# Kernel tuning notes

Hardware: AMD Instinct MI355X
Metric: run time of the kernel (lower is better)

The kernel has to match this reference:

```python
import jax, jax.numpy as jnp
import numpy as np

B, S, D, IDX = 4, 4096, 1024, 64
W = 128          # window_size
STRIDE = 64      # stride (<= W, so every query position is covered)
SPARSE = 0.5     # sparse_ratio


def setup_inputs() -> dict:
    key = jax.random.key(0)
    k1, k2, k3 = jax.random.split(key, 3)
    x = jax.random.normal(k1, (B, S, D), jnp.float32)
    wq = jax.random.normal(k2, (IDX, D), jnp.float32) * 0.02  # q_proj weight [out,in]
    wk = jax.random.normal(k3, (IDX, D), jnp.float32) * 0.02  # k_proj weight [out,in]
    return {"x": x, "wq": wq, "wk": wk}


def reference(x, wq, wk):
    # Faithful vectorization of SlidingWindowPattern.forward.
    # For every visited (start, q) pair in the original nested loops,
    # key_end = q+1 and key_start = max(0, q-W+1) are independent of `start`,
    # so the union of scatter writes equals ONE windowed top-k per query q
    # with k = max(1, int(min(q+1, W) * sparse_ratio)).
    B_, S_, _ = x.shape
    dt = x.dtype
    q = jnp.einsum('bsd,ed->bse', x, wq)
    k = jnp.einsum('bsd,ed->bse', x, wk)
    scores = jax.nn.relu(jnp.einsum('bqe,bke->bqk', q, k))  # [B,S,S]

    qpos = jnp.arange(S_)                                   # [S]
    j = jnp.arange(W)                                       # [W]
    key_idx = qpos[:, None] - (W - 1) + j[None, :]          # [S,W] absolute key positions
    valid = key_idx >= 0                                    # window is [max(0,q-W+1), q]

    gather_idx = jnp.broadcast_to(jnp.clip(key_idx, 0, S_ - 1)[None], (B_, S_, W))
    win = jnp.take_along_axis(scores, gather_idx, axis=2)   # [B,S,W]
    win = jnp.where(valid[None], win, -jnp.inf)

    order = jnp.argsort(-win, axis=-1)                      # descending; rank r -> window offset j
    win_len = jnp.minimum(qpos + 1, W)                      # number of valid keys per q
    ksel = jnp.maximum(1, jnp.floor(win_len.astype(jnp.float32) * SPARSE).astype(jnp.int32))  # [S]

    sel_key = qpos[None, :, None] - (W - 1) + order         # [B,S,W] absolute key of rank r
    write = jnp.arange(W)[None, None, :] < ksel[None, :, None]
    tgt = jnp.where(write, sel_key, S_)                     # S_ = out-of-bounds -> dropped

    mask = jnp.full((B_, S_, S_), -jnp.inf, dtype=dt)
    mask = mask.at[jnp.arange(B_)[:, None, None],
                   jnp.arange(S_)[None, :, None],
                   tgt].set(jnp.zeros((), dt), mode='drop')
    return mask[:, None]                                    # [B,1,S,S]
```

## Files before the change

### kernel.cpp

```cpp
#include <hip/hip_runtime.h>
#include <cstdint>
#include <cstddef>

#define S_LEN 4096
#define D_DIM 1024
#define NE    64
#define QB    32

typedef short short8 __attribute__((ext_vector_type(8)));
typedef float f32x4  __attribute__((ext_vector_type(4)));

__device__ __forceinline__ unsigned short f2bf(float f) {
    unsigned u = __float_as_uint(f);
    return (unsigned short)((u + 0x7FFFu + ((u >> 16) & 1u)) >> 16);
}

__global__ __launch_bounds__(256) void conv_w(
    const float* __restrict__ wq, const float* __restrict__ wk,
    unsigned short* __restrict__ whi, unsigned short* __restrict__ wlo)
{
    const int g = blockIdx.x * 256 + threadIdx.x;
    const int c = g >> 8;
    const int k = (g & 255) * 4;
    const float* src = (c < NE) ? (wq + (size_t)c * D_DIM + k)
                                : (wk + (size_t)(c - NE) * D_DIM + k);
    const float4 v = *(const float4*)src;
    unsigned short h[4], l[4];
    const float* vf = (const float*)&v;
    #pragma unroll
    for (int i = 0; i < 4; ++i) {
        h[i] = f2bf(vf[i]);
        l[i] = f2bf(vf[i] - __uint_as_float((unsigned)h[i] << 16));
    }
    *(ushort4*)(whi + (size_t)c * D_DIM + k) = make_ushort4(h[0], h[1], h[2], h[3]);
    *(ushort4*)(wlo + (size_t)c * D_DIM + k) = make_ushort4(l[0], l[1], l[2], l[3]);
}

__global__ __launch_bounds__(512) void proj_mfma(
    const float* __restrict__ x,
    const unsigned short* __restrict__ whi, const unsigned short* __restrict__ wlo,
    unsigned int* __restrict__ qhl)
{
    __shared__ __align__(16) short smem[24576];
    short* sxh = smem;
    short* sxl = smem + 4096;
    short* swh = smem + 8192;
    short* swl = smem + 16384;

    const int tid = threadIdx.x;
    const int m0  = blockIdx.x * 64;
    const int wv  = tid >> 6, l = tid & 63;
    const int mp  = wv & 1, np = wv >> 1;
    const int lrow = l & 15, lgrp = l >> 4;
    const int xr = tid >> 3, xg = tid & 7;
    const int wc = tid >> 3, wg = tid & 7;

    f32x4 acc[2][2] = {};

    for (int kb = 0; kb < D_DIM; kb += 64) {
        {
            const float* xs = x + (size_t)(m0 + xr) * D_DIM + kb + 8 * xg;
            const float4 a = *(const float4*)xs;
            const float4 b = *(const float4*)(xs + 4);
            short8 hv, lv;
            const float* af = (const float*)&a;
            const float* bf = (const float*)&b;
            #pragma unroll
            for (int i = 0; i < 4; ++i) {
                const unsigned short h0 = f2bf(af[i]);
                const unsigned short h1 = f2bf(bf[i]);
                hv[i]     = (short)h0;
                hv[i + 4] = (short)h1;
                lv[i]     = (short)f2bf(af[i] - __uint_as_float((unsigned)h0 << 16));
                lv[i + 4] = (short)f2bf(bf[i] - __uint_as_float((unsigned)h1 << 16));
            }
            const int d = xr * 64 + ((xg ^ (xr & 7)) * 8);
            *(short8*)(sxh + d) = hv;
            *(short8*)(sxl + d) = lv;
        }
        #pragma unroll
        for (int p = 0; p < 2; ++p) {
            const int c = wc + 64 * p;
            const size_t srcOff = (size_t)c * D_DIM + kb + 8 * wg;
            const int d = c * 64 + ((wg ^ (c & 7)) * 8);
            *(uint4*)(swh + d) = *(const uint4*)(whi + srcOff);
            *(uint4*)(swl + d) = *(const uint4*)(wlo + srcOff);
        }
        __syncthreads();

        short8 ah[2][2], al[2][2];
        #pragma unroll
        for (int mi = 0; mi < 2; ++mi) {
            const int ar = (2 * mp + mi) * 16 + lrow;
            #pragma unroll
            for (int kc = 0; kc < 2; ++kc) {
                const int g = kc * 4 + lgrp;
                const int o = ar * 64 + ((g ^ (ar & 7)) * 8);
                ah[mi][kc] = *(const short8*)(sxh + o);
                al[mi][kc] = *(const short8*)(sxl + o);
            }
        }
        #pragma unroll
        for (int ni = 0; ni < 2; ++ni) {
            const int bc = (2 * np + ni) * 16 + lrow;
            #pragma unroll
            for (int kc = 0; kc < 2; ++kc) {
                const int g = kc * 4 + lgrp;
                const int o = bc * 64 + ((g ^ (bc & 7)) * 8);
                const short8 bh = *(const short8*)(swh + o);
                const short8 bl = *(const short8*)(swl + o);
                #pragma unroll
                for (int mi = 0; mi < 2; ++mi) {
                    acc[mi][ni] = __builtin_amdgcn_mfma_f32_16x16x32_bf16(
                        ah[mi][kc], bh, acc[mi][ni], 0, 0, 0);
                    acc[mi][ni] = __builtin_amdgcn_mfma_f32_16x16x32_bf16(
                        al[mi][kc], bh, acc[mi][ni], 0, 0, 0);
                    acc[mi][ni] = __builtin_amdgcn_mfma_f32_16x16x32_bf16(
                        ah[mi][kc], bl, acc[mi][ni], 0, 0, 0);
                }
            }
        }
        __syncthreads();
    }

    unsigned int* tb = (unsigned int*)smem;
    #pragma unroll
    for (int mi = 0; mi < 2; ++mi)
        #pragma unroll
        for (int ni = 0; ni < 2; ++ni) {
            const int col = (2 * np + ni) * 16 + lrow;
            const int rb  = (2 * mp + mi) * 16 + lgrp * 4;
            #pragma unroll
            for (int v = 0; v < 4; ++v) {
                const float f = acc[mi][ni][v];
                const unsigned short h = f2bf(f);
                const unsigned short lo = f2bf(f - __uint_as_float((unsigned)h << 16));
                tb[(rb + v) * 128 + col] = ((unsigned)h << 16) | lo;
            }
        }
    __syncthreads();
    const uint4* tb4 = (const uint4*)tb;
    uint4* dst = (uint4*)(qhl + (size_t)m0 * 128);
    #pragma unroll
    for (int p = 0; p < 4; ++p) {
        const int i = tid + 512 * p;
        dst[i] = tb4[i];
    }
}

__global__ __launch_bounds__(512) void swp_sel(
    const unsigned int* __restrict__ qhl, unsigned short* __restrict__ outp)
{
    __shared__ __align__(16) short kmem[2 * 192 * 64];
    __shared__ __align__(16) short qmem[2 * 32 * 64];
    __shared__ __align__(16) unsigned char selb[QB * 16];
    short* kh = kmem;
    short* kl = kmem + 192 * 64;
    short* qh = qmem;
    short* ql = qmem + 32 * 64;
    unsigned long long* skey = (unsigned long long*)kmem;

    const int tid = threadIdx.x;
    const int b   = blockIdx.x >> 7;
    const int s0  = (blockIdx.x & 127) * QB;
    const size_t rowQ = (size_t)b * S_LEN + s0;

    {
        const int r = tid >> 4, c4 = tid & 15;
        const uint4 u = *(const uint4*)(qhl + (rowQ + r) * 128 + 4 * c4);
        const int off = r * 64 + (((c4 >> 1) ^ (r & 7)) * 8) + 4 * (c4 & 1);
        *(short4*)(qh + off) = make_short4((short)(u.x >> 16), (short)(u.y >> 16),
                                           (short)(u.z >> 16), (short)(u.w >> 16));
        *(short4*)(ql + off) = make_short4((short)(u.x & 0xFFFF), (short)(u.y & 0xFFFF),
                                           (short)(u.z & 0xFFFF), (short)(u.w & 0xFFFF));
    }
    #pragma unroll
    for (int p = 0; p < 5; ++p) {
        const int i = tid + 512 * p;
        const int r = i >> 4, c4 = i & 15;
        const int sk = s0 - 127 + r;
        if (r < 159 && sk >= 0) {
            const uint4 u = *(const uint4*)(qhl + ((size_t)b * S_LEN + sk) * 128 + 64 + 4 * c4);
            const int off = r * 64 + (((c4 >> 1) ^ (r & 7)) * 8) + 4 * (c4 & 1);
            *(short4*)(kh + off) = make_short4((short)(u.x >> 16), (short)(u.y >> 16),
                                               (short)(u.z >> 16), (short)(u.w >> 16));
            *(short4*)(kl + off) = make_short4((short)(u.x & 0xFFFF), (short)(u.y & 0xFFFF),
                                               (short)(u.z & 0xFFFF), (short)(u.w & 0xFFFF));
        }
    }
    __syncthreads();

    const int wv = tid >> 6, l = tid & 63;
    const int mi = wv & 1, nbase = 3 * (wv >> 1);
    const int lrow = l & 15, lgrp = l >> 4;
    f32x4 sacc[3] = {};
    {
        short8 ah[2], al[2];
        const int ar = mi * 16 + lrow;
        #pragma unroll
        for (int kc = 0; kc < 2; ++kc) {
            const int g = kc * 4 + lgrp;
            const int o = ar * 64 + ((g ^ (ar & 7)) * 8);
            ah[kc] = *(const short8*)(qh + o);
            al[kc] = *(const short8*)(ql + o);
        }
        #pragma unroll
        for (int nn = 0; nn < 3; ++nn) {
            const int bc = (nbase + nn) * 16 + lrow;
            #pragma unroll
            for (int kc = 0; kc < 2; ++kc) {
                const int g = kc * 4 + lgrp;
                const int o = bc * 64 + ((g ^ (bc & 7)) * 8);
                const short8 bh = *(const short8*)(kh + o);
                const short8 bl = *(const short8*)(kl + o);
                sacc[nn] = __builtin_amdgcn_mfma_f32_16x16x32_bf16(ah[kc], bh, sacc[nn], 0, 0, 0);
                sacc[nn] = __builtin_amdgcn_mfma_f32_16x16x32_bf16(al[kc], bh, sacc[nn], 0, 0, 0);
                sacc[nn] = __builtin_amdgcn_mfma_f32_16x16x32_bf16(ah[kc], bl, sacc[nn], 0, 0, 0);
            }
        }
    }
    __syncthreads();

    const int kvmin = 127 - s0;
    #pragma unroll
    for (int nn = 0; nn < 3; ++nn) {
        const int kidx = (nbase + nn) * 16 + lrow;
        #pragma unroll
        for (int v = 0; v < 4; ++v) {
            const int qi = mi * 16 + lgrp * 4 + v;
            const int jo = kidx - qi;
            if (jo >= 0 && jo <= 127) {
                unsigned long long key = 0ull;
                if (kidx >= kvmin) {
                    const unsigned int bits = __float_as_uint(fmaxf(sacc[nn][v], 0.0f));
                    key = ((unsigned long long)bits << 32) | (unsigned int)(159 - kidx);
                }
                skey[qi * 131 + jo] = key;
            }
        }
    }
    __syncthreads();

    {
        const int qi = tid >> 4, sl = tid & 15;
        unsigned long long th[8];
        #pragma unroll
        for (int m = 0; m < 8; ++m) th[m] = skey[qi * 131 + sl * 8 + m];
        int rk[8] = {};
        #pragma unroll 4
        for (int ii = 0; ii < 128; ++ii) {
            const unsigned long long kx = skey[qi * 131 + ii];
            #pragma unroll
            for (int m = 0; m < 8; ++m) rk[m] += (kx > th[m]) ? 1 : 0;
        }
        const int qpos = s0 + qi;
        const int wl = (qpos + 1 < 128) ? (qpos + 1) : 128;
        const int ks = ((wl >> 1) > 1) ? (wl >> 1) : 1;
        unsigned int mk = 0;
        #pragma unroll
        for (int m = 0; m < 8; ++m) if (rk[m] < ks) mk |= (1u << m);
        selb[qi * 16 + sl] = (unsigned char)mk;
    }
    __syncthreads();

    const int wb = tid >> 6, ln = tid & 63;
    #pragma unroll
    for (int rr = 0; rr < 4; ++rr) {
        const int qi = wb * 4 + rr;
        const int qpos = s0 + qi;
        const int wstart = qpos - 127;
        unsigned short* orow = outp + (rowQ + qi) * (size_t)S_LEN;
        #pragma unroll
        for (int h = 0; h < 2; ++h) {
            const int jo = ln + 64 * h;
            const int col = wstart + jo;
            if (col >= 0) {
                const int bit = (selb[qi * 16 + (jo >> 3)] >> (jo & 7)) & 1;
                orow[col] = bit ? (unsigned short)0u : (unsigned short)0xFBFFu;
            }
        }
    }
}

extern "C" void kernel_launch(void* const* d_in, const int* in_sizes, int n_in,
                              void* d_out, int out_size, void* d_ws, size_t ws_size,
                              hipStream_t stream)
{
    (void)in_sizes; (void)n_in; (void)out_size; (void)ws_size;
    const float* x  = (const float*)d_in[0];
    const float* wq = (const float*)d_in[1];
    const float* wk = (const float*)d_in[2];
    unsigned short* out = (unsigned short*)d_out;

    unsigned int* qhl = (unsigned int*)d_ws;
    unsigned short* whi = (unsigned short*)((char*)d_ws + ((size_t)8 << 20));
    unsigned short* wlo = whi + (size_t)128 * D_DIM;

    conv_w<<<128, 256, 0, stream>>>(wq, wk, whi, wlo);
    proj_mfma<<<256, 512, 0, stream>>>(x, whi, wlo, qhl);
    swp_sel<<<512, 512, 0, stream>>>(qhl, out);
}
```

Before: 61.10 us.

## Fuse weight bf16 split into projection and store q/k as split hi/lo planes

Removes the separate conv_w launch by converting fp32 weights to bf16 hi/lo pairs inside the projection kernel's tile loader. The projection output changes from packed hi|lo words to two separate planes, so the selection kernel can copy 16-byte chunks straight into shared memory without unpacking. It also changes the skey row stride from 131 to 132 and processes two keys per rank-loop iteration. Each projection block now redoes the weight conversion, adding extra ALU work and fp32 weight traffic in exchange for one fewer launch.

```diff
diff --git a/kernel.cpp b/kernel.cpp
--- a/kernel.cpp
+++ b/kernel.cpp
@@ -15,31 +15,10 @@
     return (unsigned short)((u + 0x7FFFu + ((u >> 16) & 1u)) >> 16);
 }
 
-__global__ __launch_bounds__(256) void conv_w(
-    const float* __restrict__ wq, const float* __restrict__ wk,
-    unsigned short* __restrict__ whi, unsigned short* __restrict__ wlo)
-{
-    const int g = blockIdx.x * 256 + threadIdx.x;
-    const int c = g >> 8;
-    const int k = (g & 255) * 4;
-    const float* src = (c < NE) ? (wq + (size_t)c * D_DIM + k)
-                                : (wk + (size_t)(c - NE) * D_DIM + k);
-    const float4 v = *(const float4*)src;
-    unsigned short h[4], l[4];
-    const float* vf = (const float*)&v;
-    #pragma unroll
-    for (int i = 0; i < 4; ++i) {
-        h[i] = f2bf(vf[i]);
-        l[i] = f2bf(vf[i] - __uint_as_float((unsigned)h[i] << 16));
-    }
-    *(ushort4*)(whi + (size_t)c * D_DIM + k) = make_ushort4(h[0], h[1], h[2], h[3]);
-    *(ushort4*)(wlo + (size_t)c * D_DIM + k) = make_ushort4(l[0], l[1], l[2], l[3]);
-}
-
 __global__ __launch_bounds__(512) void proj_mfma(
     const float* __restrict__ x,
-    const unsigned short* __restrict__ whi, const unsigned short* __restrict__ wlo,
-    unsigned int* __restrict__ qhl)
+    const float* __restrict__ wq, const float* __restrict__ wk,
+    unsigned short* __restrict__ qhi, unsigned short* __restrict__ qlo)
 {
     __shared__ __align__(16) short smem[24576];
     short* sxh = smem;
@@ -81,10 +60,24 @@
         #pragma unroll
         for (int p = 0; p < 2; ++p) {
             const int c = wc + 64 * p;
-            const size_t srcOff = (size_t)c * D_DIM + kb + 8 * wg;
+            const float* wsrc = (p ? wk : wq) + (size_t)wc * D_DIM + kb + 8 * wg;
+            const float4 a = *(const float4*)wsrc;
+            const float4 b = *(const float4*)(wsrc + 4);
+            short8 hv, lv;
+            const float* af = (const float*)&a;
+            const float* bf = (const float*)&b;
+            #pragma unroll
+            for (int i = 0; i < 4; ++i) {
+                const unsigned short h0 = f2bf(af[i]);
+                const unsigned short h1 = f2bf(bf[i]);
+                hv[i]     = (short)h0;
+                hv[i + 4] = (short)h1;
+                lv[i]     = (short)f2bf(af[i] - __uint_as_float((unsigned)h0 << 16));
+                lv[i + 4] = (short)f2bf(bf[i] - __uint_as_float((unsigned)h1 << 16));
+            }
             const int d = c * 64 + ((wg ^ (c & 7)) * 8);
-            *(uint4*)(swh + d) = *(const uint4*)(whi + srcOff);
-            *(uint4*)(swl + d) = *(const uint4*)(wlo + srcOff);
+            *(short8*)(swh + d) = hv;
+            *(short8*)(swl + d) = lv;
         }
         __syncthreads();
 
@@ -140,16 +133,24 @@
         }
     __syncthreads();
     const uint4* tb4 = (const uint4*)tb;
-    uint4* dst = (uint4*)(qhl + (size_t)m0 * 128);
     #pragma unroll
     for (int p = 0; p < 4; ++p) {
         const int i = tid + 512 * p;
-        dst[i] = tb4[i];
+        const uint4 u = tb4[i];
+        const int row = i >> 5, c4 = (i & 31) * 4;
+        const size_t off = (size_t)(m0 + row) * 128 + c4;
+        *(ushort4*)(qhi + off) = make_ushort4(
+            (unsigned short)(u.x >> 16), (unsigned short)(u.y >> 16),
+            (unsigned short)(u.z >> 16), (unsigned short)(u.w >> 16));
+        *(ushort4*)(qlo + off) = make_ushort4(
+            (unsigned short)(u.x & 0xFFFF), (unsigned short)(u.y & 0xFFFF),
+            (unsigned short)(u.z & 0xFFFF), (unsigned short)(u.w & 0xFFFF));
     }
 }
 
 __global__ __launch_bounds__(512) void swp_sel(
-    const unsigned int* __restrict__ qhl, unsigned short* __restrict__ outp)
+    const unsigned short* __restrict__ qhi, const unsigned short* __restrict__ qlo,
+    unsigned short* __restrict__ outp)
 {
     __shared__ __align__(16) short kmem[2 * 192 * 64];
     __shared__ __align__(16) short qmem[2 * 32 * 64];
@@ -166,26 +167,24 @@
     const size_t rowQ = (size_t)b * S_LEN + s0;
 
     {
-        const int r = tid >> 4, c4 = tid & 15;
-        const uint4 u = *(const uint4*)(qhl + (rowQ + r) * 128 + 4 * c4);
-        const int off = r * 64 + (((c4 >> 1) ^ (r & 7)) * 8) + 4 * (c4 & 1);
-        *(short4*)(qh + off) = make_short4((short)(u.x >> 16), (short)(u.y >> 16),
-                                           (short)(u.z >> 16), (short)(u.w >> 16));
-        *(short4*)(ql + off) = make_short4((short)(u.x & 0xFFFF), (short)(u.y & 0xFFFF),
-                                           (short)(u.z & 0xFFFF), (short)(u.w & 0xFFFF));
+        const int plane = tid >> 8;
+        const int r = (tid >> 3) & 31, g = tid & 7;
+        const unsigned short* src = (plane ? qlo : qhi) + (rowQ + r) * 128 + 8 * g;
+        short* dst = (plane ? ql : qh) + r * 64 + ((g ^ (r & 7)) * 8);
+        *(short8*)dst = *(const short8*)src;
     }
     #pragma unroll
     for (int p = 0; p < 5; ++p) {
         const int i = tid + 512 * p;
-        const int r = i >> 4, c4 = i & 15;
+        const int r = i >> 4;
+        const int g = (i >> 1) & 7;
+        const int plane = i & 1;
         const int sk = s0 - 127 + r;
         if (r < 159 && sk >= 0) {
-            const uint4 u = *(const uint4*)(qhl + ((size_t)b * S_LEN + sk) * 128 + 64 + 4 * c4);
-            const int off = r * 64 + (((c4 >> 1) ^ (r & 7)) * 8) + 4 * (c4 & 1);
-            *(short4*)(kh + off) = make_short4((short)(u.x >> 16), (short)(u.y >> 16),
-                                               (short)(u.z >> 16), (short)(u.w >> 16));
-            *(short4*)(kl + off) = make_short4((short)(u.x & 0xFFFF), (short)(u.y & 0xFFFF),
-                                               (short)(u.z & 0xFFFF), (short)(u.w & 0xFFFF));
+            const unsigned short* src = (plane ? qlo : qhi)
+                                      + ((size_t)b * S_LEN + sk) * 128 + 64 + 8 * g;
+            short* dst = (plane ? kl : kh) + r * 64 + ((g ^ (r & 7)) * 8);
+            *(short8*)dst = *(const short8*)src;
         }
     }
     __syncthreads();
@@ -235,7 +234,7 @@
                     const unsigned int bits = __float_as_uint(fmaxf(sacc[nn][v], 0.0f));
                     key = ((unsigned long long)bits << 32) | (unsigned int)(159 - kidx);
                 }
-                skey[qi * 131 + jo] = key;
+                skey[qi * 132 + jo] = key;
             }
         }
     }
@@ -245,13 +244,15 @@
         const int qi = tid >> 4, sl = tid & 15;
         unsigned long long th[8];
         #pragma unroll
-        for (int m = 0; m < 8; ++m) th[m] = skey[qi * 131 + sl * 8 + m];
+        for (int m = 0; m < 8; ++m) th[m] = skey[qi * 132 + sl * 8 + m];
         int rk[8] = {};
         #pragma unroll 4
-        for (int ii = 0; ii < 128; ++ii) {
-            const unsigned long long kx = skey[qi * 131 + ii];
-            #pragma unroll
-            for (int m = 0; m < 8; ++m) rk[m] += (kx > th[m]) ? 1 : 0;
+        for (int ii = 0; ii < 128; ii += 2) {
+            const unsigned long long k0 = skey[qi * 132 + ii];
+            const unsigned long long k1 = skey[qi * 132 + ii + 1];
+            #pragma unroll
+            for (int m = 0; m < 8; ++m)
+                rk[m] += ((k0 > th[m]) ? 1 : 0) + ((k1 > th[m]) ? 1 : 0);
         }
         const int qpos = s0 + qi;
         const int wl = (qpos + 1 < 128) ? (qpos + 1) : 128;
@@ -292,11 +293,9 @@
     const float* wk = (const float*)d_in[2];
     unsigned short* out = (unsigned short*)d_out;
 
-    unsigned int* qhl = (unsigned int*)d_ws;
-    unsigned short* whi = (unsigned short*)((char*)d_ws + ((size_t)8 << 20));
-    unsigned short* wlo = whi + (size_t)128 * D_DIM;
-
-    conv_w<<<128, 256, 0, stream>>>(wq, wk, whi, wlo);
-    proj_mfma<<<256, 512, 0, stream>>>(x, whi, wlo, qhl);
-    swp_sel<<<512, 512, 0, stream>>>(qhl, out);
+    unsigned short* qhi = (unsigned short*)d_ws;
+    unsigned short* qlo = qhi + (size_t)16384 * 128;
+
+    proj_mfma<<<256, 512, 0, stream>>>(x, wq, wk, qhi, qlo);
+    swp_sel<<<512, 512, 0, stream>>>(qhi, qlo, out);
 }
```

Measured after the change: 64.40 us. 1.05x slower.
